# Kernel optimization log

Measured on AMD Instinct MI355X. Metric: run time of the kernel, lower is better.

Reference implementation:

```python
import jax, jax.numpy as jnp
import numpy as np

B, S, D = 1, 4096, 1024
H, Dh = 16, 64
F = 4096  # mlp_factor * D
EPS = 1e-6


def _ln(x, scale, bias=None):
    m = jnp.mean(x, axis=-1, keepdims=True)
    v = jnp.var(x, axis=-1, keepdims=True)
    y = (x - m) * jax.lax.rsqrt(v + EPS) * scale
    return y + bias if bias is not None else y


def setup_inputs() -> dict:
    key = jax.random.key(0)
    ks = jax.random.split(key, 10)
    lecun = lambda k, shape, fan_in: (jax.random.normal(k, shape, jnp.float32) * (fan_in ** -0.5))
    inp = {
        "x": jax.random.normal(ks[0], (B, S, D), jnp.float32),
        # causal mask, broadcastable to [B, H, S, S]
        "mask": jnp.tril(jnp.ones((S, S), bool))[None, None],
        # PreNorm (TPNorm -> LayerNorm)
        "ln_scale": jnp.ones((D,), jnp.float32),
        "ln_bias": jnp.zeros((D,), jnp.float32),
        # MLP input projection
        "w_in": lecun(ks[1], (D, F), D),
        "b_in": jnp.zeros((F,), jnp.float32),
        # QKV projection
        "wq": lecun(ks[2], (D, H, Dh), D),
        "bq": jnp.zeros((H, Dh), jnp.float32),
        "wk": lecun(ks[3], (D, H, Dh), D),
        "bk": jnp.zeros((H, Dh), jnp.float32),
        "wv": lecun(ks[4], (D, H, Dh), D),
        "bv": jnp.zeros((H, Dh), jnp.float32),
        # qk-norm scales (normalize_qk=True)
        "qn_scale": jnp.ones((Dh,), jnp.float32),
        "kn_scale": jnp.ones((Dh,), jnp.float32),
        # MLP output projection
        "w_mo": lecun(ks[5], (F, D), F),
        "b_mo": jnp.zeros((D,), jnp.float32),
        # Attention output projection
        "w_ao": lecun(ks[6], (H * Dh, D), H * Dh),
        "b_ao": jnp.zeros((D,), jnp.float32),
    }
    return inp


def reference(x, mask, ln_scale, ln_bias, w_in, b_in, wq, bq, wk, bk, wv, bv,
              qn_scale, kn_scale, w_mo, b_mo, w_ao, b_ao):
    residual = x
    xn = _ln(x, ln_scale, ln_bias)

    # fused QKV + MLP-input projections (QKVMLPDenseParallel)
    h = jax.nn.gelu(jnp.einsum("bsd,df->bsf", xn, w_in) + b_in)  # [B,S,F]
    q = jnp.einsum("bsd,dhk->bshk", xn, wq) + bq  # [B,S,H,Dh]
    k = jnp.einsum("bsd,dhk->bshk", xn, wk) + bk
    v = jnp.einsum("bsd,dhk->bshk", xn, wv) + bv
    # normalize_qk: per-head LayerNorm (no bias) on q, k
    q = _ln(q, qn_scale)
    k = _ln(k, kn_scale)

    # dot-product attention
    scores = jnp.einsum("bqhd,bkhd->bhqk", q, k) / np.sqrt(Dh).astype(np.float32)
    scores = jnp.where(mask, scores, jnp.finfo(scores.dtype).min)
    attn = jax.nn.softmax(scores, axis=-1)
    o = jnp.einsum("bhqk,bkhd->bqhd", attn, v)  # [B,S,H,Dh]

    # fused attention-out + MLP-out projections (AttnMLPOutParallel)
    mlp_out = jnp.einsum("bsf,fd->bsd", h, w_mo) + b_mo
    attn_out = jnp.einsum("bse,ed->bsd", o.reshape(B, S, H * Dh), w_ao) + b_ao

    # dropout deterministic (train=False); residual add
    return residual + mlp_out + attn_out
```

## Files before the change

kernel.cpp:

```cpp
#include <hip/hip_runtime.h>
#include <hip/hip_fp16.h>

typedef _Float16 half8 __attribute__((ext_vector_type(8)));
typedef float floatx4 __attribute__((ext_vector_type(4)));

constexpr int kS = 4096;
constexpr int kD = 1024;
constexpr int kH = 16;
constexpr int kDh = 64;
constexpr int kF = 4096;
constexpr int kNQKV = kF + 3 * kD;
constexpr int kKOut = kF + kD;

__device__ __forceinline__ void async_ld16(const void* g, void* l) {
  __builtin_amdgcn_global_load_lds(
      (const __attribute__((address_space(1))) void*)g,
      (__attribute__((address_space(3))) void*)l, 16, 0, 0);
}

__global__ __launch_bounds__(256) void wtrans_kernel(
    const float* __restrict__ src, _Float16* __restrict__ dst,
    int N, int dldk, int noff, int koff) {
  __shared__ float t[32][33];
  const int tid = threadIdx.x;
  const int n0 = blockIdx.x * 32, k0 = blockIdx.y * 32;
#pragma unroll
  for (int i = 0; i < 4; ++i) {
    const int kl = (tid >> 5) + i * 8, nl = tid & 31;
    t[kl][nl] = src[(size_t)(k0 + kl) * N + n0 + nl];
  }
  __syncthreads();
#pragma unroll
  for (int i = 0; i < 4; ++i) {
    const int nl = (tid >> 5) + i * 8, kl = tid & 31;
    dst[(size_t)(noff + n0 + nl) * dldk + koff + k0 + kl] = (_Float16)t[kl][nl];
  }
}

__global__ __launch_bounds__(256) void htrans_kernel(
    const _Float16* __restrict__ src, _Float16* __restrict__ dst, int R, int C) {
  __shared__ _Float16 t[32][34];
  const int tid = threadIdx.x;
  const int c0 = blockIdx.x * 32, r0 = blockIdx.y * 32;
#pragma unroll
  for (int i = 0; i < 4; ++i) {
    const int rl = (tid >> 5) + i * 8, cl = tid & 31;
    t[rl][cl] = src[(size_t)(r0 + rl) * C + c0 + cl];
  }
  __syncthreads();
#pragma unroll
  for (int i = 0; i < 4; ++i) {
    const int cl = (tid >> 5) + i * 8, rl = tid & 31;
    dst[(size_t)(c0 + cl) * R + r0 + rl] = t[rl][cl];
  }
}

__global__ __launch_bounds__(256) void biasprep_kernel(
    const float* b_in, const float* bq, const float* bk, const float* bv,
    const float* b_mo, const float* b_ao, float* bcat, float* bsum) {
  const int i = blockIdx.x * 256 + threadIdx.x;
  if (i < kF) bcat[i] = b_in[i];
  else if (i < kF + kD) bcat[i] = bq[i - kF];
  else if (i < kF + 2 * kD) bcat[i] = bk[i - kF - kD];
  else if (i < kNQKV) bcat[i] = bv[i - kF - 2 * kD];
  else if (i < kNQKV + kD) bsum[i - kNQKV] = b_mo[i - kNQKV] + b_ao[i - kNQKV];
}

__global__ __launch_bounds__(256) void ln_kernel(
    const float* __restrict__ x, const float* __restrict__ scale,
    const float* __restrict__ bias, _Float16* __restrict__ xn) {
  const int row = blockIdx.x;
  const int tid = threadIdx.x;
  const float* xr = x + (size_t)row * kD;
  float v[4];
  float s = 0.f, sq = 0.f;
#pragma unroll
  for (int i = 0; i < 4; ++i) {
    v[i] = xr[tid + 256 * i];
    s += v[i];
    sq += v[i] * v[i];
  }
  for (int off = 32; off; off >>= 1) {
    s += __shfl_xor(s, off);
    sq += __shfl_xor(sq, off);
  }
  __shared__ float red[8];
  const int wv = tid >> 6;
  if ((tid & 63) == 0) { red[wv] = s; red[wv + 4] = sq; }
  __syncthreads();
  s = red[0] + red[1] + red[2] + red[3];
  sq = red[4] + red[5] + red[6] + red[7];
  const float mean = s * (1.0f / kD);
  const float var = sq * (1.0f / kD) - mean * mean;
  const float rstd = rsqrtf(var + 1e-6f);
#pragma unroll
  for (int i = 0; i < 4; ++i) {
    int d = tid + 256 * i;
    xn[(size_t)row * kD + d] = (_Float16)((v[i] - mean) * rstd * scale[d] + bias[d]);
  }
}

__global__ __launch_bounds__(256) void qknorm_kernel(
    _Float16* __restrict__ t, const float* __restrict__ scale, float smul) {
  const int row = (blockIdx.x << 2) + (threadIdx.x >> 6);
  const int lane = threadIdx.x & 63;
  _Float16* tr = t + (size_t)row * kDh;
  const float val = (float)tr[lane];
  float s = val;
  for (int off = 32; off; off >>= 1) s += __shfl_xor(s, off);
  const float mean = s * (1.0f / kDh);
  const float dv = val - mean;
  float sq = dv * dv;
  for (int off = 32; off; off >>= 1) sq += __shfl_xor(sq, off);
  const float rstd = rsqrtf(sq * (1.0f / kDh) + 1e-6f);
  tr[lane] = (_Float16)(dv * rstd * scale[lane] * smul);
}

__device__ __forceinline__ float fast_gelu(float xv) {
  const float z = 0.7978845608028654f * (xv + 0.044715f * xv * xv * xv);
  const float u = exp2f(fminf(2.885390081777927f * z, 80.0f));
  return xv * u / (1.0f + u);
}

__global__ __launch_bounds__(256) void gemm_qkvin(
    const _Float16* __restrict__ A, const _Float16* __restrict__ Bp,
    const float* __restrict__ bcat, _Float16* __restrict__ ho,
    _Float16* __restrict__ q, _Float16* __restrict__ k, _Float16* __restrict__ v) {
  __shared__ alignas(16) _Float16 Ts[16 * 512];
  _Float16* As = Ts;
  _Float16* Bs = Ts + 8 * 512;

  const int tid = threadIdx.x;
  const int lane = tid & 63;
  const int wave = tid >> 6;
  const int wm = (wave >> 1) * 64;
  const int wn = (wave & 1) * 64;
  const int m0 = blockIdx.x * 128;
  const int n0 = blockIdx.y * 128;
  const int lrow = lane & 15;
  const int quad = lane >> 4;

  floatx4 acc[4][4] = {};

  for (int k0 = 0; k0 < kD; k0 += 32) {
    __syncthreads();
#pragma unroll
    for (int i = 0; i < 4; ++i) {
      const int chunk = wave * 4 + i;
      const int r = ((chunk & 7) << 4) + (lane >> 2);
      const int csrc = ((lane & 3) ^ ((r >> 1) & 3)) << 3;
      const _Float16* src = (chunk < 8)
          ? A + (size_t)(m0 + r) * kD + k0 + csrc
          : Bp + (size_t)(n0 + r) * kD + k0 + csrc;
      async_ld16(src, Ts + chunk * 512);
    }
    __syncthreads();

    half8 af[4], bf[4];
#pragma unroll
    for (int i = 0; i < 4; ++i) {
      const int ra = wm + i * 16 + lrow;
      const int rb = wn + i * 16 + lrow;
      af[i] = *reinterpret_cast<const half8*>(&As[ra * 32 + ((quad ^ ((ra >> 1) & 3)) << 3)]);
      bf[i] = *reinterpret_cast<const half8*>(&Bs[rb * 32 + ((quad ^ ((rb >> 1) & 3)) << 3)]);
    }
#pragma unroll
    for (int i = 0; i < 4; ++i)
#pragma unroll
      for (int j = 0; j < 4; ++j)
        acc[i][j] = __builtin_amdgcn_mfma_f32_16x16x32_f16(af[i], bf[j], acc[i][j], 0, 0, 0);
  }

#pragma unroll
  for (int i = 0; i < 4; ++i) {
    const int gm = m0 + wm + i * 16 + quad * 4;
#pragma unroll
    for (int j = 0; j < 4; ++j) {
      const int gn = n0 + wn + j * 16 + lrow;
      const float bn = bcat[gn];
#pragma unroll
      for (int r = 0; r < 4; ++r) {
        float vv = acc[i][j][r] + bn;
        if (gn < kF) {
          ho[(size_t)(gm + r) * kKOut + gn] = (_Float16)fast_gelu(vv);
        } else {
          const int reg = gn - kF;
          _Float16* dst = (reg < kD) ? q : (reg < 2 * kD) ? k : v;
          dst[(size_t)(gm + r) * kD + (reg & (kD - 1))] = (_Float16)vv;
        }
      }
    }
  }
}

__global__ __launch_bounds__(256) void initout_kernel(
    const float* __restrict__ x, const float* __restrict__ bsum,
    float* __restrict__ out) {
  const int i = blockIdx.x * 256 + threadIdx.x;
  out[i] = x[i] + bsum[i & (kD - 1)];
}

__global__ __launch_bounds__(256) void gemm_out(
    const _Float16* __restrict__ A, const _Float16* __restrict__ Bp,
    float* __restrict__ out) {
  __shared__ alignas(16) _Float16 Ts[16 * 512];
  _Float16* As = Ts;
  _Float16* Bs = Ts + 8 * 512;

  const int tid = threadIdx.x;
  const int lane = tid & 63;
  const int wave = tid >> 6;
  const int wm = (wave >> 1) * 64;
  const int wn = (wave & 1) * 64;
  const int m0 = blockIdx.x * 128;
  const int n0 = blockIdx.y * 128;
  const int kbeg = blockIdx.z * (kKOut / 2);
  const int lrow = lane & 15;
  const int quad = lane >> 4;

  floatx4 acc[4][4] = {};

  for (int k0 = kbeg; k0 < kbeg + kKOut / 2; k0 += 32) {
    __syncthreads();
#pragma unroll
    for (int i = 0; i < 4; ++i) {
      const int chunk = wave * 4 + i;
      const int r = ((chunk & 7) << 4) + (lane >> 2);
      const int csrc = ((lane & 3) ^ ((r >> 1) & 3)) << 3;
      const _Float16* src = (chunk < 8)
          ? A + (size_t)(m0 + r) * kKOut + k0 + csrc
          : Bp + (size_t)(n0 + r) * kKOut + k0 + csrc;
      async_ld16(src, Ts + chunk * 512);
    }
    __syncthreads();

    half8 af[4], bf[4];
#pragma unroll
    for (int i = 0; i < 4; ++i) {
      const int ra = wm + i * 16 + lrow;
      const int rb = wn + i * 16 + lrow;
      af[i] = *reinterpret_cast<const half8*>(&As[ra * 32 + ((quad ^ ((ra >> 1) & 3)) << 3)]);
      bf[i] = *reinterpret_cast<const half8*>(&Bs[rb * 32 + ((quad ^ ((rb >> 1) & 3)) << 3)]);
    }
#pragma unroll
    for (int i = 0; i < 4; ++i)
#pragma unroll
      for (int j = 0; j < 4; ++j)
        acc[i][j] = __builtin_amdgcn_mfma_f32_16x16x32_f16(af[i], bf[j], acc[i][j], 0, 0, 0);
  }

#pragma unroll
  for (int i = 0; i < 4; ++i) {
    const int gm = m0 + wm + i * 16 + quad * 4;
#pragma unroll
    for (int j = 0; j < 4; ++j) {
      const int gn = n0 + wn + j * 16 + lrow;
#pragma unroll
      for (int r = 0; r < 4; ++r)
        atomicAdd(out + (size_t)(gm + r) * kD + gn, acc[i][j][r]);
    }
  }
}

__global__ __launch_bounds__(256) void zeroacc_kernel(float* __restrict__ p, int n) {
  const int i = blockIdx.x * 256 + threadIdx.x;
  if (i < n) p[i] = 0.f;
}

__global__ __launch_bounds__(256) void fattn_kernel(
    const _Float16* __restrict__ Q, const _Float16* __restrict__ K,
    const _Float16* __restrict__ Vt, float* __restrict__ Oacc,
    float* __restrict__ Lacc) {
  __shared__ alignas(16) _Float16 Qs[64 * 64];
  __shared__ alignas(16) _Float16 Ks[64 * 64];
  __shared__ alignas(16) _Float16 Vs[64 * 64];
  __shared__ alignas(16) _Float16 Ps[64 * 72];

  const int tid = threadIdx.x;
  const int lane = tid & 63;
  const int wave = tid >> 6;
  const int lrow = lane & 15;
  const int quad = lane >> 4;
  const int h = blockIdx.y;
  const int pair = blockIdx.x;
  const int split = blockIdx.z;

  const int rs = lane >> 3;
  const int cs = lane & 7;
  constexpr float kOff = 11.5415603f;

  for (int pass = 0; pass < 2; ++pass) {
    const int qtile = pass ? (63 - pair) : pair;
    const int qbase = qtile * 64;

    __syncthreads();
#pragma unroll
    for (int i = 0; i < 2; ++i) {
      const int chunk = wave * 2 + i;
      const int r = chunk * 8 + rs;
      async_ld16(Q + (size_t)(qbase + r) * kD + h * kDh + ((cs ^ (r & 7)) << 3),
                 Qs + chunk * 512);
    }
    __syncthreads();

    half8 qf[2];
#pragma unroll
    for (int kt = 0; kt < 2; ++kt)
      qf[kt] = *reinterpret_cast<const half8*>(
          &Qs[(wave * 16 + lrow) * 64 + (((kt * 4 + quad) ^ (lrow & 7)) << 3)]);

    float lst[4] = {0.f, 0.f, 0.f, 0.f};
    floatx4 oacc[4] = {};
    const int qw = qbase + wave * 16;

    for (int t = split; t <= qtile; t += 2) {
      const int k0 = t * 64;
      __syncthreads();
#pragma unroll
      for (int i = 0; i < 4; ++i) {
        const int id = wave * 4 + i;
        if (id < 8) {
          const int r = id * 8 + rs;
          async_ld16(K + (size_t)(k0 + r) * kD + h * kDh + ((cs ^ (r & 7)) << 3),
                     Ks + id * 512);
        } else {
          const int c = id - 8;
          const int r = c * 8 + rs;
          async_ld16(Vt + (size_t)(h * kDh + r) * kS + k0 + ((cs ^ (r & 7)) << 3),
                     Vs + c * 512);
        }
      }
      __syncthreads();

      const bool diag = (t == qtile);

      floatx4 sacc[4] = {};
#pragma unroll
      for (int jt = 0; jt < 4; ++jt) {
        if (diag && jt > wave) continue;
#pragma unroll
        for (int kt = 0; kt < 2; ++kt) {
          const int rb = jt * 16 + lrow;
          half8 bfk = *reinterpret_cast<const half8*>(
              &Ks[rb * 64 + (((kt * 4 + quad) ^ (lrow & 7)) << 3)]);
          sacc[jt] = __builtin_amdgcn_mfma_f32_16x16x32_f16(qf[kt], bfk, sacc[jt], 0, 0, 0);
        }
      }

      if (diag) {
#pragma unroll
        for (int jt = 0; jt < 4; ++jt) {
          const int kg = k0 + jt * 16 + lrow;
#pragma unroll
          for (int r = 0; r < 4; ++r)
            if (kg > qw + quad * 4 + r) sacc[jt][r] = -1e30f;
        }
      }

#pragma unroll
      for (int jt = 0; jt < 4; ++jt)
#pragma unroll
        for (int r = 0; r < 4; ++r) {
          const float p = exp2f(sacc[jt][r] - kOff);
          sacc[jt][r] = p;
          lst[r] += p;
        }

#pragma unroll
      for (int jt = 0; jt < 4; ++jt)
#pragma unroll
        for (int r = 0; r < 4; ++r)
          Ps[(wave * 16 + quad * 4 + r) * 72 + jt * 16 + lrow] = (_Float16)sacc[jt][r];

      const int ktmax = (diag && wave < 2) ? 1 : 2;
      for (int kt = 0; kt < ktmax; ++kt) {
        half8 pf = *reinterpret_cast<const half8*>(
            &Ps[(wave * 16 + lrow) * 72 + (kt * 4 + quad) * 8]);
#pragma unroll
        for (int jt = 0; jt < 4; ++jt) {
          const int rb = jt * 16 + lrow;
          half8 vf = *reinterpret_cast<const half8*>(
              &Vs[rb * 64 + (((kt * 4 + quad) ^ (lrow & 7)) << 3)]);
          oacc[jt] = __builtin_amdgcn_mfma_f32_16x16x32_f16(pf, vf, oacc[jt], 0, 0, 0);
        }
      }
    }

#pragma unroll
    for (int r = 0; r < 4; ++r) {
#pragma unroll
      for (int off = 8; off; off >>= 1) lst[r] += __shfl_xor(lst[r], off);
    }
#pragma unroll
    for (int r = 0; r < 4; ++r) {
      const int qg = qw + quad * 4 + r;
      if (lrow == 0) atomicAdd(Lacc + qg * kH + h, lst[r]);
#pragma unroll
      for (int jt = 0; jt < 4; ++jt)
        atomicAdd(Oacc + ((size_t)qg * kH + h) * kDh + jt * 16 + lrow, oacc[jt][r]);
    }
  }
}

__global__ __launch_bounds__(256) void norm_kernel(
    const float* __restrict__ Oacc, const float* __restrict__ Lacc,
    _Float16* __restrict__ ho) {
  const int idx = blockIdx.x * 256 + threadIdx.x;
  const int q = idx >> 10, rem = idx & 1023;
  const float l = Lacc[(q << 4) + (rem >> 6)];
  ho[(size_t)q * kKOut + kF + rem] = (_Float16)(Oacc[idx] / l);
}

extern "C" void kernel_launch(void* const* d_in, const int* in_sizes, int n_in,
                              void* d_out, int out_size, void* d_ws, size_t ws_size,
                              hipStream_t stream) {
  const float* x        = (const float*)d_in[0];
  const float* ln_scale = (const float*)d_in[2];
  const float* ln_bias  = (const float*)d_in[3];
  const float* w_in     = (const float*)d_in[4];
  const float* b_in     = (const float*)d_in[5];
  const float* wq       = (const float*)d_in[6];
  const float* bq       = (const float*)d_in[7];
  const float* wk       = (const float*)d_in[8];
  const float* bk       = (const float*)d_in[9];
  const float* wv       = (const float*)d_in[10];
  const float* bv       = (const float*)d_in[11];
  const float* qn_scale = (const float*)d_in[12];
  const float* kn_scale = (const float*)d_in[13];
  const float* w_mo     = (const float*)d_in[14];
  const float* b_mo     = (const float*)d_in[15];
  const float* w_ao     = (const float*)d_in[16];
  const float* b_ao     = (const float*)d_in[17];
  float* out = (float*)d_out;

  char* ws = (char*)d_ws;
  size_t off = 0;
  auto alloc = [&](size_t bytes) { char* p = ws + off; off += bytes; return p; };
  char* zone = (char*)alloc((size_t)kS * kD * 2 + (size_t)kNQKV * kD * 2);
  _Float16* xn   = (_Float16*)zone;
  _Float16* Wqkv = (_Float16*)(zone + (size_t)kS * kD * 2);
  float* Oacc = (float*)zone;
  float* Lacc = (float*)(zone + (size_t)kS * kD * 4);
  _Float16* Wout = (_Float16*)alloc((size_t)kD * kKOut * 2);
  float*    bcat = (float*)alloc((size_t)kNQKV * 4);
  float*    bsum = (float*)alloc((size_t)kD * 4);
  _Float16* ho   = (_Float16*)alloc((size_t)kS * kKOut * 2);
  _Float16* q_h  = (_Float16*)alloc((size_t)kS * kD * 2);
  _Float16* k_h  = (_Float16*)alloc((size_t)kS * kD * 2);
  _Float16* v_h  = (_Float16*)alloc((size_t)kS * kD * 2);
  _Float16* v_t  = (_Float16*)alloc((size_t)kS * kD * 2);

  wtrans_kernel<<<dim3(kF / 32, kD / 32), 256, 0, stream>>>(w_in, Wqkv, kF, kD, 0, 0);
  wtrans_kernel<<<dim3(kD / 32, kD / 32), 256, 0, stream>>>(wq, Wqkv, kD, kD, kF, 0);
  wtrans_kernel<<<dim3(kD / 32, kD / 32), 256, 0, stream>>>(wk, Wqkv, kD, kD, kF + kD, 0);
  wtrans_kernel<<<dim3(kD / 32, kD / 32), 256, 0, stream>>>(wv, Wqkv, kD, kD, kF + 2 * kD, 0);
  wtrans_kernel<<<dim3(kD / 32, kF / 32), 256, 0, stream>>>(w_mo, Wout, kD, kKOut, 0, 0);
  wtrans_kernel<<<dim3(kD / 32, kD / 32), 256, 0, stream>>>(w_ao, Wout, kD, kKOut, 0, kF);

  biasprep_kernel<<<(kNQKV + kD + 255) / 256, 256, 0, stream>>>(
      b_in, bq, bk, bv, b_mo, b_ao, bcat, bsum);

  ln_kernel<<<kS, 256, 0, stream>>>(x, ln_scale, ln_bias, xn);

  gemm_qkvin<<<dim3(kS / 128, kNQKV / 128), 256, 0, stream>>>(
      xn, Wqkv, bcat, ho, q_h, k_h, v_h);

  qknorm_kernel<<<kS * kH / 4, 256, 0, stream>>>(q_h, qn_scale, 0.18033688f);
  qknorm_kernel<<<kS * kH / 4, 256, 0, stream>>>(k_h, kn_scale, 1.0f);

  htrans_kernel<<<dim3(kD / 32, kS / 32), 256, 0, stream>>>(v_h, v_t, kS, kD);

  zeroacc_kernel<<<(kS * kD + kS * kH + 255) / 256, 256, 0, stream>>>(
      Oacc, kS * kD + kS * kH);

  fattn_kernel<<<dim3(32, kH, 2), 256, 0, stream>>>(q_h, k_h, v_t, Oacc, Lacc);

  norm_kernel<<<kS * kD / 256, 256, 0, stream>>>(Oacc, Lacc, ho);

  initout_kernel<<<kS * kD / 256, 256, 0, stream>>>(x, bsum, out);
  gemm_out<<<dim3(kS / 128, kD / 128, 2), 256, 0, stream>>>(ho, Wout, out);
}
```

Before: 494.5 us.

## Fuse qk-norm into QKV GEMM epilogue, merge weight transposes, retile attention

Merges the six weight-transpose launches into one kernel that dispatches on block index. Moves the per-head q/k LayerNorm into the QKV GEMM epilogue, using wave shuffles across the 64-column head slice and dropping two qknorm passes over global memory. Retiles flash attention to 128-row query tiles per block with two 16-row fragments per wave, splits the key range three ways, and maps blocks so heads are grouped by XCD. This adds register pressure and LDS use in attention, plus some idle blocks on skipped key tiles.

```diff
diff --git a/kernel.cpp b/kernel.cpp
--- a/kernel.cpp
+++ b/kernel.cpp
@@ -18,12 +18,22 @@
       (__attribute__((address_space(3))) void*)l, 16, 0, 0);
 }
 
-__global__ __launch_bounds__(256) void wtrans_kernel(
-    const float* __restrict__ src, _Float16* __restrict__ dst,
-    int N, int dldk, int noff, int koff) {
+__global__ __launch_bounds__(256) void wtrans_all(
+    const float* __restrict__ w_in, const float* __restrict__ wq,
+    const float* __restrict__ wk, const float* __restrict__ wv,
+    const float* __restrict__ w_mo, const float* __restrict__ w_ao,
+    _Float16* __restrict__ Wqkv, _Float16* __restrict__ Wout) {
   __shared__ float t[32][33];
+  int id = blockIdx.x;
+  const float* src; _Float16* dst; int N, ldk, noff, koff, nt, kt;
+  if (id < 4096)       { src = w_in; dst = Wqkv; N = kF; ldk = kD; noff = 0;        koff = 0;  nt = id & 127; kt = id >> 7; }
+  else if (id < 5120)  { id -= 4096; src = wq;  dst = Wqkv; N = kD; ldk = kD; noff = kF;       koff = 0;  nt = id & 31; kt = id >> 5; }
+  else if (id < 6144)  { id -= 5120; src = wk;  dst = Wqkv; N = kD; ldk = kD; noff = kF + kD;  koff = 0;  nt = id & 31; kt = id >> 5; }
+  else if (id < 7168)  { id -= 6144; src = wv;  dst = Wqkv; N = kD; ldk = kD; noff = kF + 2*kD; koff = 0; nt = id & 31; kt = id >> 5; }
+  else if (id < 11264) { id -= 7168; src = w_mo; dst = Wout; N = kD; ldk = kKOut; noff = 0;    koff = 0;  nt = id & 31; kt = id >> 5; }
+  else                 { id -= 11264; src = w_ao; dst = Wout; N = kD; ldk = kKOut; noff = 0;   koff = kF; nt = id & 31; kt = id >> 5; }
   const int tid = threadIdx.x;
-  const int n0 = blockIdx.x * 32, k0 = blockIdx.y * 32;
+  const int n0 = nt * 32, k0 = kt * 32;
 #pragma unroll
   for (int i = 0; i < 4; ++i) {
     const int kl = (tid >> 5) + i * 8, nl = tid & 31;
@@ -33,7 +43,7 @@
 #pragma unroll
   for (int i = 0; i < 4; ++i) {
     const int nl = (tid >> 5) + i * 8, kl = tid & 31;
-    dst[(size_t)(noff + n0 + nl) * dldk + koff + k0 + kl] = (_Float16)t[kl][nl];
+    dst[(size_t)(noff + n0 + nl) * ldk + koff + k0 + kl] = (_Float16)t[kl][nl];
   }
 }
 
@@ -100,22 +110,6 @@
   }
 }
 
-__global__ __launch_bounds__(256) void qknorm_kernel(
-    _Float16* __restrict__ t, const float* __restrict__ scale, float smul) {
-  const int row = (blockIdx.x << 2) + (threadIdx.x >> 6);
-  const int lane = threadIdx.x & 63;
-  _Float16* tr = t + (size_t)row * kDh;
-  const float val = (float)tr[lane];
-  float s = val;
-  for (int off = 32; off; off >>= 1) s += __shfl_xor(s, off);
-  const float mean = s * (1.0f / kDh);
-  const float dv = val - mean;
-  float sq = dv * dv;
-  for (int off = 32; off; off >>= 1) sq += __shfl_xor(sq, off);
-  const float rstd = rsqrtf(sq * (1.0f / kDh) + 1e-6f);
-  tr[lane] = (_Float16)(dv * rstd * scale[lane] * smul);
-}
-
 __device__ __forceinline__ float fast_gelu(float xv) {
   const float z = 0.7978845608028654f * (xv + 0.044715f * xv * xv * xv);
   const float u = exp2f(fminf(2.885390081777927f * z, 80.0f));
@@ -124,7 +118,8 @@
 
 __global__ __launch_bounds__(256) void gemm_qkvin(
     const _Float16* __restrict__ A, const _Float16* __restrict__ Bp,
-    const float* __restrict__ bcat, _Float16* __restrict__ ho,
+    const float* __restrict__ bcat, const float* __restrict__ qn_scale,
+    const float* __restrict__ kn_scale, _Float16* __restrict__ ho,
     _Float16* __restrict__ q, _Float16* __restrict__ k, _Float16* __restrict__ v) {
   __shared__ alignas(16) _Float16 Ts[16 * 512];
   _Float16* As = Ts;
@@ -171,22 +166,65 @@
         acc[i][j] = __builtin_amdgcn_mfma_f32_16x16x32_f16(af[i], bf[j], acc[i][j], 0, 0, 0);
   }
 
-#pragma unroll
-  for (int i = 0; i < 4; ++i) {
-    const int gm = m0 + wm + i * 16 + quad * 4;
-#pragma unroll
-    for (int j = 0; j < 4; ++j) {
-      const int gn = n0 + wn + j * 16 + lrow;
-      const float bn = bcat[gn];
+  const int nblk = n0 + wn;
+  if (nblk < kF) {
+#pragma unroll
+    for (int i = 0; i < 4; ++i) {
+      const int gm = m0 + wm + i * 16 + quad * 4;
+#pragma unroll
+      for (int j = 0; j < 4; ++j) {
+        const int gn = nblk + j * 16 + lrow;
+        const float bn = bcat[gn];
+#pragma unroll
+        for (int r = 0; r < 4; ++r)
+          ho[(size_t)(gm + r) * kKOut + gn] = (_Float16)fast_gelu(acc[i][j][r] + bn);
+      }
+    }
+  } else if (nblk >= kF + 2 * kD) {
+#pragma unroll
+    for (int i = 0; i < 4; ++i) {
+      const int gm = m0 + wm + i * 16 + quad * 4;
+#pragma unroll
+      for (int j = 0; j < 4; ++j) {
+        const int gn = nblk + j * 16 + lrow;
+        const float bn = bcat[gn];
+#pragma unroll
+        for (int r = 0; r < 4; ++r)
+          v[(size_t)(gm + r) * kD + ((gn - kF) & (kD - 1))] = (_Float16)(acc[i][j][r] + bn);
+      }
+    }
+  } else {
+    const bool isq = nblk < kF + kD;
+    const float* nsc = isq ? qn_scale : kn_scale;
+    const float sm = isq ? 0.18033688f : 1.0f;
+    _Float16* dst = isq ? q : k;
+    const int col0 = (nblk - kF) & (kD - 1);
+    float bj[4];
+#pragma unroll
+    for (int j = 0; j < 4; ++j) bj[j] = bcat[nblk + j * 16 + lrow];
+#pragma unroll
+    for (int i = 0; i < 4; ++i) {
+      const int gm = m0 + wm + i * 16 + quad * 4;
 #pragma unroll
       for (int r = 0; r < 4; ++r) {
-        float vv = acc[i][j][r] + bn;
-        if (gn < kF) {
-          ho[(size_t)(gm + r) * kKOut + gn] = (_Float16)fast_gelu(vv);
-        } else {
-          const int reg = gn - kF;
-          _Float16* dst = (reg < kD) ? q : (reg < 2 * kD) ? k : v;
-          dst[(size_t)(gm + r) * kD + (reg & (kD - 1))] = (_Float16)vv;
+        float vals[4], s1 = 0.f, s2 = 0.f;
+#pragma unroll
+        for (int j = 0; j < 4; ++j) {
+          const float vv = acc[i][j][r] + bj[j];
+          vals[j] = vv; s1 += vv; s2 += vv * vv;
+        }
+#pragma unroll
+        for (int off = 1; off <= 8; off <<= 1) {
+          s1 += __shfl_xor(s1, off);
+          s2 += __shfl_xor(s2, off);
+        }
+        const float mean = s1 * (1.0f / 64.0f);
+        const float rstd = rsqrtf(s2 * (1.0f / 64.0f) - mean * mean + 1e-6f);
+#pragma unroll
+        for (int j = 0; j < 4; ++j) {
+          const int d = j * 16 + lrow;
+          dst[(size_t)(gm + r) * kD + col0 + d] =
+              (_Float16)((vals[j] - mean) * rstd * nsc[d] * sm);
         }
       }
     }
@@ -271,60 +309,70 @@
     const _Float16* __restrict__ Q, const _Float16* __restrict__ K,
     const _Float16* __restrict__ Vt, float* __restrict__ Oacc,
     float* __restrict__ Lacc) {
-  __shared__ alignas(16) _Float16 Qs[64 * 64];
+  __shared__ alignas(16) _Float16 Qs[128 * 64];
   __shared__ alignas(16) _Float16 Ks[64 * 64];
   __shared__ alignas(16) _Float16 Vs[64 * 64];
-  __shared__ alignas(16) _Float16 Ps[64 * 72];
+  __shared__ alignas(16) _Float16 Ps[128 * 72];
 
   const int tid = threadIdx.x;
   const int lane = tid & 63;
   const int wave = tid >> 6;
   const int lrow = lane & 15;
   const int quad = lane >> 4;
-  const int h = blockIdx.y;
-  const int pair = blockIdx.x;
-  const int split = blockIdx.z;
+
+  const int id = blockIdx.x;
+  const int xcd = id & 7;
+  const int idx = id >> 3;
+  const int h = (xcd << 1) | (idx & 1);
+  const int rem = idx >> 1;
+  const int pair = rem & 15;
+  const int split = rem >> 4;
 
   const int rs = lane >> 3;
   const int cs = lane & 7;
   constexpr float kOff = 11.5415603f;
 
   for (int pass = 0; pass < 2; ++pass) {
-    const int qtile = pass ? (63 - pair) : pair;
-    const int qbase = qtile * 64;
+    const int qtile = pass ? (31 - pair) : pair;
+    const int qbase = qtile * 128;
 
     __syncthreads();
 #pragma unroll
-    for (int i = 0; i < 2; ++i) {
-      const int chunk = wave * 2 + i;
+    for (int i = 0; i < 4; ++i) {
+      const int chunk = wave * 4 + i;
       const int r = chunk * 8 + rs;
       async_ld16(Q + (size_t)(qbase + r) * kD + h * kDh + ((cs ^ (r & 7)) << 3),
                  Qs + chunk * 512);
     }
     __syncthreads();
 
-    half8 qf[2];
-#pragma unroll
-    for (int kt = 0; kt < 2; ++kt)
-      qf[kt] = *reinterpret_cast<const half8*>(
-          &Qs[(wave * 16 + lrow) * 64 + (((kt * 4 + quad) ^ (lrow & 7)) << 3)]);
-
-    float lst[4] = {0.f, 0.f, 0.f, 0.f};
-    floatx4 oacc[4] = {};
-    const int qw = qbase + wave * 16;
-
-    for (int t = split; t <= qtile; t += 2) {
+    half8 qf[2][2];
+#pragma unroll
+    for (int i = 0; i < 2; ++i)
+#pragma unroll
+      for (int kt = 0; kt < 2; ++kt) {
+        const int row = wave * 32 + i * 16 + lrow;
+        qf[i][kt] = *reinterpret_cast<const half8*>(
+            &Qs[row * 64 + (((kt * 4 + quad) ^ (row & 7)) << 3)]);
+      }
+
+    float lst[2][4] = {};
+    floatx4 oacc[2][4] = {};
+    const int qw = qbase + wave * 32;
+    const int tmax = 2 * qtile + 1;
+
+    for (int t = split; t <= tmax; t += 3) {
       const int k0 = t * 64;
       __syncthreads();
 #pragma unroll
       for (int i = 0; i < 4; ++i) {
-        const int id = wave * 4 + i;
-        if (id < 8) {
-          const int r = id * 8 + rs;
+        const int c2 = wave * 4 + i;
+        if (c2 < 8) {
+          const int r = c2 * 8 + rs;
           async_ld16(K + (size_t)(k0 + r) * kD + h * kDh + ((cs ^ (r & 7)) << 3),
-                     Ks + id * 512);
+                     Ks + c2 * 512);
         } else {
-          const int c = id - 8;
+          const int c = c2 - 8;
           const int r = c * 8 + rs;
           async_ld16(Vt + (size_t)(h * kDh + r) * kS + k0 + ((cs ^ (r & 7)) << 3),
                      Vs + c * 512);
@@ -332,73 +380,89 @@
       }
       __syncthreads();
 
-      const bool diag = (t == qtile);
-
-      floatx4 sacc[4] = {};
+      if (k0 > qw + 31) continue;
+
+      const bool diag = (k0 + 63 > qw);
+      floatx4 sacc[2][4] = {};
 #pragma unroll
       for (int jt = 0; jt < 4; ++jt) {
-        if (diag && jt > wave) continue;
+        if (diag && (k0 + jt * 16 > qw + 31)) continue;
 #pragma unroll
         for (int kt = 0; kt < 2; ++kt) {
           const int rb = jt * 16 + lrow;
           half8 bfk = *reinterpret_cast<const half8*>(
-              &Ks[rb * 64 + (((kt * 4 + quad) ^ (lrow & 7)) << 3)]);
-          sacc[jt] = __builtin_amdgcn_mfma_f32_16x16x32_f16(qf[kt], bfk, sacc[jt], 0, 0, 0);
+              &Ks[rb * 64 + (((kt * 4 + quad) ^ (rb & 7)) << 3)]);
+          sacc[0][jt] = __builtin_amdgcn_mfma_f32_16x16x32_f16(qf[0][kt], bfk, sacc[0][jt], 0, 0, 0);
+          sacc[1][jt] = __builtin_amdgcn_mfma_f32_16x16x32_f16(qf[1][kt], bfk, sacc[1][jt], 0, 0, 0);
         }
       }
 
       if (diag) {
 #pragma unroll
-        for (int jt = 0; jt < 4; ++jt) {
-          const int kg = k0 + jt * 16 + lrow;
+        for (int i = 0; i < 2; ++i)
+#pragma unroll
+          for (int jt = 0; jt < 4; ++jt) {
+            const int kg = k0 + jt * 16 + lrow;
+#pragma unroll
+            for (int r = 0; r < 4; ++r)
+              if (kg > qw + i * 16 + quad * 4 + r) sacc[i][jt][r] = -1e30f;
+          }
+      }
+
+#pragma unroll
+      for (int i = 0; i < 2; ++i)
+#pragma unroll
+        for (int jt = 0; jt < 4; ++jt)
+#pragma unroll
+          for (int r = 0; r < 4; ++r) {
+            const float p = exp2f(sacc[i][jt][r] - kOff);
+            sacc[i][jt][r] = p;
+            lst[i][r] += p;
+          }
+
+#pragma unroll
+      for (int i = 0; i < 2; ++i)
+#pragma unroll
+        for (int jt = 0; jt < 4; ++jt)
 #pragma unroll
           for (int r = 0; r < 4; ++r)
-            if (kg > qw + quad * 4 + r) sacc[jt][r] = -1e30f;
-        }
-      }
-
-#pragma unroll
-      for (int jt = 0; jt < 4; ++jt)
-#pragma unroll
-        for (int r = 0; r < 4; ++r) {
-          const float p = exp2f(sacc[jt][r] - kOff);
-          sacc[jt][r] = p;
-          lst[r] += p;
-        }
-
-#pragma unroll
-      for (int jt = 0; jt < 4; ++jt)
-#pragma unroll
-        for (int r = 0; r < 4; ++r)
-          Ps[(wave * 16 + quad * 4 + r) * 72 + jt * 16 + lrow] = (_Float16)sacc[jt][r];
-
-      const int ktmax = (diag && wave < 2) ? 1 : 2;
+            Ps[(wave * 32 + i * 16 + quad * 4 + r) * 72 + jt * 16 + lrow] =
+                (_Float16)sacc[i][jt][r];
+
+      const int ktmax = (k0 >= qw) ? 1 : 2;
       for (int kt = 0; kt < ktmax; ++kt) {
-        half8 pf = *reinterpret_cast<const half8*>(
-            &Ps[(wave * 16 + lrow) * 72 + (kt * 4 + quad) * 8]);
+        half8 pf[2];
+#pragma unroll
+        for (int i = 0; i < 2; ++i)
+          pf[i] = *reinterpret_cast<const half8*>(
+              &Ps[(wave * 32 + i * 16 + lrow) * 72 + (kt * 4 + quad) * 8]);
 #pragma unroll
         for (int jt = 0; jt < 4; ++jt) {
           const int rb = jt * 16 + lrow;
           half8 vf = *reinterpret_cast<const half8*>(
-              &Vs[rb * 64 + (((kt * 4 + quad) ^ (lrow & 7)) << 3)]);
-          oacc[jt] = __builtin_amdgcn_mfma_f32_16x16x32_f16(pf, vf, oacc[jt], 0, 0, 0);
+              &Vs[rb * 64 + (((kt * 4 + quad) ^ (rb & 7)) << 3)]);
+          oacc[0][jt] = __builtin_amdgcn_mfma_f32_16x16x32_f16(pf[0], vf, oacc[0][jt], 0, 0, 0);
+          oacc[1][jt] = __builtin_amdgcn_mfma_f32_16x16x32_f16(pf[1], vf, oacc[1][jt], 0, 0, 0);
         }
       }
     }
 
 #pragma unroll
-    for (int r = 0; r < 4; ++r) {
-#pragma unroll
-      for (int off = 8; off; off >>= 1) lst[r] += __shfl_xor(lst[r], off);
-    }
-#pragma unroll
-    for (int r = 0; r < 4; ++r) {
-      const int qg = qw + quad * 4 + r;
-      if (lrow == 0) atomicAdd(Lacc + qg * kH + h, lst[r]);
-#pragma unroll
-      for (int jt = 0; jt < 4; ++jt)
-        atomicAdd(Oacc + ((size_t)qg * kH + h) * kDh + jt * 16 + lrow, oacc[jt][r]);
-    }
+    for (int i = 0; i < 2; ++i)
+#pragma unroll
+      for (int r = 0; r < 4; ++r)
+#pragma unroll
+        for (int off = 8; off; off >>= 1) lst[i][r] += __shfl_xor(lst[i][r], off);
+#pragma unroll
+    for (int i = 0; i < 2; ++i)
+#pragma unroll
+      for (int r = 0; r < 4; ++r) {
+        const int qg = qw + i * 16 + quad * 4 + r;
+        if (lrow == 0) atomicAdd(Lacc + qg * kH + h, lst[i][r]);
+#pragma unroll
+        for (int jt = 0; jt < 4; ++jt)
+          atomicAdd(Oacc + ((size_t)qg * kH + h) * kDh + jt * 16 + lrow, oacc[i][jt][r]);
+      }
   }
 }
 
@@ -450,30 +514,20 @@
   _Float16* v_h  = (_Float16*)alloc((size_t)kS * kD * 2);
   _Float16* v_t  = (_Float16*)alloc((size_t)kS * kD * 2);
 
-  wtrans_kernel<<<dim3(kF / 32, kD / 32), 256, 0, stream>>>(w_in, Wqkv, kF, kD, 0, 0);
-  wtrans_kernel<<<dim3(kD / 32, kD / 32), 256, 0, stream>>>(wq, Wqkv, kD, kD, kF, 0);
-  wtrans_kernel<<<dim3(kD / 32, kD / 32), 256, 0, stream>>>(wk, Wqkv, kD, kD, kF + kD, 0);
-  wtrans_kernel<<<dim3(kD / 32, kD / 32), 256, 0, stream>>>(wv, Wqkv, kD, kD, kF + 2 * kD, 0);
-  wtrans_kernel<<<dim3(kD / 32, kF / 32), 256, 0, stream>>>(w_mo, Wout, kD, kKOut, 0, 0);
-  wtrans_kernel<<<dim3(kD / 32, kD / 32), 256, 0, stream>>>(w_ao, Wout, kD, kKOut, 0, kF);
-
+  wtrans_all<<<12288, 256, 0, stream>>>(w_in, wq, wk, wv, w_mo, w_ao, Wqkv, Wout);
   biasprep_kernel<<<(kNQKV + kD + 255) / 256, 256, 0, stream>>>(
       b_in, bq, bk, bv, b_mo, b_ao, bcat, bsum);
-
   ln_kernel<<<kS, 256, 0, stream>>>(x, ln_scale, ln_bias, xn);
 
   gemm_qkvin<<<dim3(kS / 128, kNQKV / 128), 256, 0, stream>>>(
-      xn, Wqkv, bcat, ho, q_h, k_h, v_h);
-
-  qknorm_kernel<<<kS * kH / 4, 256, 0, stream>>>(q_h, qn_scale, 0.18033688f);
-  qknorm_kernel<<<kS * kH / 4, 256, 0, stream>>>(k_h, kn_scale, 1.0f);
+      xn, Wqkv, bcat, qn_scale, kn_scale, ho, q_h, k_h, v_h);
 
   htrans_kernel<<<dim3(kD / 32, kS / 32), 256, 0, stream>>>(v_h, v_t, kS, kD);
 
   zeroacc_kernel<<<(kS * kD + kS * kH + 255) / 256, 256, 0, stream>>>(
       Oacc, kS * kD + kS * kH);
 
-  fattn_kernel<<<dim3(32, kH, 2), 256, 0, stream>>>(q_h, k_h, v_t, Oacc, Lacc);
+  fattn_kernel<<<768, 256, 0, stream>>>(q_h, k_h, v_t, Oacc, Lacc);
 
   norm_kernel<<<kS * kD / 256, 256, 0, stream>>>(Oacc, Lacc, ho);
 
```

Measured after the change: 494.1 us. No clear change (-0.1%).
